# Kernel tuning notes

Measured on AMD Instinct MI355X. Metric: run time of the kernel, lower is better.

## Reference

```python
import jax, jax.numpy as jnp
import numpy as np

NEG_SLOPE = 0.2
EPS = 1e-16

N_NODES = 10000
N_EDGES = 80000
F_IN = 128
HID = 300
H1 = 5  # first_heads
H3 = 3  # out_head
N_CLASSES = 40


def gat_conv(x, edge_index, W, att_src, att_dst, bias, heads, out_ch, concat):
    """PyG-style GATConv (v1 attention), eval mode (no dropout).

    x: [N, F_in]; edge_index: [2, E] (row 0 = source, row 1 = target),
    self-loops already included. W: [F_in, heads*out_ch];
    att_src/att_dst: [heads, out_ch].
    """
    N = x.shape[0]
    h = (x @ W).reshape(N, heads, out_ch)            # [N, H, C]
    a_src = jnp.einsum('nhc,hc->nh', h, att_src)     # [N, H]
    a_dst = jnp.einsum('nhc,hc->nh', h, att_dst)     # [N, H]
    src, dst = edge_index[0], edge_index[1]
    e = jax.nn.leaky_relu(a_src[src] + a_dst[dst], NEG_SLOPE)  # [E, H]
    # segment softmax over incoming edges of each target node
    m = jax.ops.segment_max(e, dst, num_segments=N)  # [N, H]
    ex = jnp.exp(e - m[dst])
    s = jax.ops.segment_sum(ex, dst, num_segments=N)
    alpha = ex / (s[dst] + EPS)                      # [E, H]
    msg = h[src] * alpha[:, :, None]                 # [E, H, C]
    out = jax.ops.segment_sum(msg, dst, num_segments=N)  # [N, H, C]
    if concat:
        out = out.reshape(N, heads * out_ch)
    else:
        out = out.mean(axis=1)
    return out + bias


def setup_inputs() -> dict:
    key = jax.random.key(0)
    ks = jax.random.split(key, 12)
    glorot = lambda k, shape: jax.random.normal(k, shape, jnp.float32) * np.sqrt(
        2.0 / (shape[0] + shape[-1]))
    x = jax.random.normal(ks[0], (N_NODES, F_IN), jnp.float32)
    edge_index = jax.random.randint(ks[1], (2, N_EDGES), 0, N_NODES, jnp.int64)
    return {
        'x': x,
        'edge_index': edge_index,
        'W1': glorot(ks[2], (F_IN, H1 * HID)),
        'as1': glorot(ks[3], (H1, HID)),
        'ad1': glorot(ks[4], (H1, HID)),
        'b1': jnp.zeros((H1 * HID,), jnp.float32),
        'W2': glorot(ks[5], (H1 * HID, H1 * HID)),
        'as2': glorot(ks[6], (H1, HID)),
        'ad2': glorot(ks[7], (H1, HID)),
        'b2': jnp.zeros((H1 * HID,), jnp.float32),
        'W3': glorot(ks[8], (H1 * HID, H3 * N_CLASSES)),
        'as3': glorot(ks[9], (H3, N_CLASSES)),
        'ad3': glorot(ks[10], (H3, N_CLASSES)),
        'b3': jnp.zeros((N_CLASSES,), jnp.float32),
    }


def reference(x, edge_index, W1, as1, ad1, b1, W2, as2, ad2, b2, W3, as3, ad3, b3):
    N = x.shape[0]
    # PyG GATConv adds self-loops by default
    loops = jnp.arange(N, dtype=edge_index.dtype)
    ei = jnp.concatenate([edge_index, jnp.stack([loops, loops])], axis=1)
    # dropout layers are identity in eval mode
    h = gat_conv(x, ei, W1, as1, ad1, b1, H1, HID, True)
    h = jax.nn.elu(h)
    h2 = gat_conv(h, ei, W2, as2, ad2, b2, H1, HID, True)
    h = jax.nn.elu(h + h2)
    h = gat_conv(h, ei, W3, as3, ad3, b3, H3, N_CLASSES, False)  # [N, n_cls]
    pooled = h.sum(axis=0, keepdims=True)                        # [1, n_cls]
    return (pooled, jax.nn.log_softmax(pooled, axis=1))
```

## Files before the change

### kernel.cpp

```cpp
#include <hip/hip_runtime.h>
#include <hip/hip_bf16.h>
#include <math.h>

#define NN       10000
#define F_IN     128
#define HID      300
#define H1       5
#define H3       3
#define NCLS     40
#define HC1      (H1*HID)
#define KPAD     1536
#define HS12     304
#define NL12     1520
#define HS3      48
#define NL3      144
#define LD3      160
#define NEG_SLOPE 0.2f
#define EPSV     1e-16f

typedef __attribute__((ext_vector_type(8))) short bf16x8;
typedef __attribute__((ext_vector_type(8))) unsigned short u16x8;
typedef __attribute__((ext_vector_type(4))) float f32x4;

__device__ inline unsigned short f2bf(float f) {
  unsigned int u = __builtin_bit_cast(unsigned int, f);
  unsigned int r = (u + 0x7FFFu + ((u >> 16) & 1u)) >> 16;
  return (unsigned short)r;
}
__device__ inline float bf2f(unsigned short s) {
  unsigned int u = ((unsigned int)s) << 16;
  return __builtin_bit_cast(float, u);
}

__device__ __forceinline__ void gl2lds16(const unsigned short* g, unsigned short* l) {
  __builtin_amdgcn_global_load_lds(
      (const __attribute__((address_space(1))) unsigned int*)(const void*)g,
      (__attribute__((address_space(3))) unsigned int*)(void*)l, 16, 0, 0);
}

__global__ void k_count(const int* __restrict__ ei, int* __restrict__ counts,
                        int E0, int Etot) {
  int e = blockIdx.x * 256 + threadIdx.x;
  if (e >= Etot) return;
  int dst = (e < E0) ? ei[E0 + e] : (e - E0);
  atomicAdd(&counts[dst], 1);
}

__global__ __launch_bounds__(256) void k_scan(const int* __restrict__ counts,
                                              int* __restrict__ offsets,
                                              int* __restrict__ cursor,
                                              int N, int Etot) {
  __shared__ int sh[256];
  const int CH = 40;
  int t = threadIdx.x;
  int base = t * CH;
  int s = 0;
  for (int i = 0; i < CH; i++) {
    int idx = base + i;
    if (idx < N) s += counts[idx];
  }
  sh[t] = s;
  __syncthreads();
  for (int d = 1; d < 256; d <<= 1) {
    int v = (t >= d) ? sh[t - d] : 0;
    __syncthreads();
    sh[t] += v;
    __syncthreads();
  }
  int run = sh[t] - s;
  for (int i = 0; i < CH; i++) {
    int idx = base + i;
    if (idx < N) {
      offsets[idx] = run;
      cursor[idx] = run;
      run += counts[idx];
    }
  }
  if (t == 0) offsets[N] = Etot;
}

__global__ void k_scatter(const int* __restrict__ ei, int* __restrict__ cursor,
                          int* __restrict__ csr_src, int E0, int Etot) {
  int e = blockIdx.x * 256 + threadIdx.x;
  if (e >= Etot) return;
  int src, dst;
  if (e < E0) { src = ei[e]; dst = ei[E0 + e]; }
  else        { src = dst = e - E0; }
  int pos = atomicAdd(&cursor[dst], 1);
  csr_src[pos] = src;
}

__global__ void k_cvt(const float* __restrict__ in, unsigned short* __restrict__ out,
                      int R, int C, int Cpad) {
  long long idx = (long long)blockIdx.x * 256 + threadIdx.x;
  if (idx >= (long long)R * Cpad) return;
  int r = (int)(idx / Cpad), c = (int)(idx - (long long)r * Cpad);
  out[idx] = (c < C) ? f2bf(in[(size_t)r * C + c]) : 0;
}

__global__ void k_attpad3(const float* __restrict__ as1, const float* __restrict__ ad1,
                          const float* __restrict__ as2, const float* __restrict__ ad2,
                          const float* __restrict__ as3, const float* __restrict__ ad3,
                          float* __restrict__ ps1, float* __restrict__ pd1,
                          float* __restrict__ ps2, float* __restrict__ pd2,
                          float* __restrict__ ps3, float* __restrict__ pd3) {
  int i = blockIdx.x * 256 + threadIdx.x;
  if (i < KPAD) {
    int h = i / HS12, cin = i - h * HS12;
    bool live = (h < H1) && (cin < HID);
    int o = live ? (h * HID + cin) : 0;
    ps1[i] = live ? as1[o] : 0.f;
    pd1[i] = live ? ad1[o] : 0.f;
    ps2[i] = live ? as2[o] : 0.f;
    pd2[i] = live ? ad2[o] : 0.f;
  }
  if (i < LD3) {
    int h = i / HS3, cin = i - h * HS3;
    bool live = (h < H3) && (cin < NCLS);
    ps3[i] = live ? as3[h * NCLS + cin] : 0.f;
    pd3[i] = live ? ad3[h * NCLS + cin] : 0.f;
  }
}

__global__ __launch_bounds__(256) void k_cvtT(const float* __restrict__ in,
                                              unsigned short* __restrict__ out,
                                              int K, int Nm, int kC, int kS, int Kp,
                                              int nC, int nS, int Nmp) {
  __shared__ float tile[64][65];
  int k0 = blockIdx.y * 64, n0 = blockIdx.x * 64;
  int c = threadIdx.x & 63, r = threadIdx.x >> 6;
  for (int rr = r; rr < 64; rr += 4) {
    int kp = k0 + rr;
    int np = n0 + c;
    float v = 0.f;
    if (kp < Kp && np < Nmp) {
      int ck = kp % kS, bk = kp / kS;
      int cn = np % nS, bn_ = np / nS;
      int ko = bk * kC + ck, no = bn_ * nC + cn;
      if (ck < kC && ko < K && cn < nC && no < Nm) v = in[(size_t)ko * Nm + no];
    }
    tile[rr][c] = v;
  }
  __syncthreads();
  for (int rr = r; rr < 64; rr += 4) {
    int np = n0 + rr, kp = k0 + c;
    if (np < Nmp && kp < Kp) out[(size_t)np * Kp + kp] = f2bf(tile[c][rr]);
  }
}

#define BM 256
#define BN 128
#define BK 64

__global__ __launch_bounds__(512) void gemm_mfma(
    const unsigned short* __restrict__ A,
    const unsigned short* __restrict__ Bt,
    unsigned short* __restrict__ Cbf,
    int M, int Kpad, int Nmat, int ldc, int klen, int nT,
    float* __restrict__ Cacc) {
  __shared__ unsigned short As[BM * BK];
  __shared__ unsigned short Bs[BN * BK];
  int tid = threadIdx.x;
  int lane = tid & 63, wid = tid >> 6;
  int wm = wid >> 1, wn = wid & 1;
  int bid = blockIdx.x;
  int slot = bid & 7, idx = bid >> 3;
  int nTi = idx % nT, mg = idx / nT;
  int bm = (slot + 8 * mg) * BM, bn = nTi * BN;
  int quad = lane >> 4, l16 = lane & 15;
  int kq = quad * 8;
  int koff = blockIdx.y * klen;

  int ar0 = min(bm + 32 * wid + l16, M - 1);
  int ar1 = min(bm + 32 * wid + 16 + l16, M - 1);
  int br0 = min(bn + 16 * wid + l16, Nmat - 1);
  const unsigned short* gA0 = A + (size_t)ar0 * Kpad + kq;
  const unsigned short* gA1 = A + (size_t)ar1 * Kpad + kq;
  const unsigned short* gB0 = Bt + (size_t)br0 * Kpad + kq;
  unsigned short* lA = As + 4 * wid * 512;
  unsigned short* lB = Bs + 2 * wid * 512;

  f32x4 acc[4][4] = {};

  for (int kt = koff; kt < koff + klen; kt += BK) {
    gl2lds16(gA0 + kt,      lA);
    gl2lds16(gA0 + kt + 32, lA + 512);
    gl2lds16(gA1 + kt,      lA + 1024);
    gl2lds16(gA1 + kt + 32, lA + 1536);
    gl2lds16(gB0 + kt,      lB);
    gl2lds16(gB0 + kt + 32, lB + 512);
    __syncthreads();
#pragma unroll
    for (int kh = 0; kh < 2; kh++) {
      bf16x8 af[4], bfr[4];
#pragma unroll
      for (int i = 0; i < 4; i++) {
        af[i]  = *(const bf16x8*)(As + ((wm * 4 + i) * 2 + kh) * 512 + lane * 8);
        bfr[i] = *(const bf16x8*)(Bs + ((wn * 4 + i) * 2 + kh) * 512 + lane * 8);
      }
#pragma unroll
      for (int i = 0; i < 4; i++)
#pragma unroll
        for (int j = 0; j < 4; j++)
          acc[i][j] = __builtin_amdgcn_mfma_f32_16x16x32_bf16(af[i], bfr[j], acc[i][j], 0, 0, 0);
    }
    __syncthreads();
  }

#pragma unroll
  for (int i = 0; i < 4; i++) {
    int rowb = bm + wm * 64 + i * 16 + quad * 4;
#pragma unroll
    for (int j = 0; j < 4; j++) {
      int col = bn + wn * 64 + j * 16 + l16;
      if (col < ldc) {
        bool live = col < Nmat;
        if (Cacc) {
#pragma unroll
          for (int r = 0; r < 4; r++) {
            int row = rowb + r;
            if (live && row < M) atomicAdd(&Cacc[(size_t)row * ldc + col], acc[i][j][r]);
          }
        } else {
#pragma unroll
          for (int r = 0; r < 4; r++) {
            int row = rowb + r;
            if (row < M) Cbf[(size_t)row * ldc + col] = live ? f2bf(acc[i][j][r]) : 0;
          }
        }
      }
    }
  }
}

__global__ void k_att(unsigned short* __restrict__ hfeat, int ldh,
                      const float* __restrict__ attp_s,
                      const float* __restrict__ attp_d,
                      float* __restrict__ asrc, float* __restrict__ adst,
                      int H, int HS, const float* __restrict__ Cacc, int Nlive) {
  int n = blockIdx.x, t = threadIdx.x;
  __shared__ float s_ps[8], s_pd[8];
  if (t < 8) { s_ps[t] = 0.f; s_pd[t] = 0.f; }
  __syncthreads();
  int col0 = t * 8;
  if (col0 < ldh) {
    int hj = col0 / HS;
    float ps = 0.f, pd = 0.f;
    if (Cacc) {
      const float4* p = (const float4*)(Cacc + (size_t)n * ldh + col0);
      float4 f0 = p[0], f1 = p[1];
      float fv[8] = {f0.x, f0.y, f0.z, f0.w, f1.x, f1.y, f1.z, f1.w};
      u16x8 st;
#pragma unroll
      for (int j = 0; j < 8; j++) {
        bool live = (col0 + j) < Nlive;
        float v = live ? fv[j] : 0.f;
        st[j] = live ? f2bf(v) : 0;
        ps += v * attp_s[col0 + j];
        pd += v * attp_d[col0 + j];
      }
      *(u16x8*)(hfeat + (size_t)n * ldh + col0) = st;
    } else {
      u16x8 rv = *(const u16x8*)(hfeat + (size_t)n * ldh + col0);
#pragma unroll
      for (int j = 0; j < 8; j++) {
        float v = bf2f(rv[j]);
        ps += v * attp_s[col0 + j];
        pd += v * attp_d[col0 + j];
      }
    }
    atomicAdd(&s_ps[hj], ps);
    atomicAdd(&s_pd[hj], pd);
  }
  __syncthreads();
  if (t < H) {
    asrc[(size_t)n * H + t] = s_ps[t];
    adst[(size_t)n * H + t] = s_pd[t];
  }
}

__global__ __launch_bounds__(64) void k_agg(
    const unsigned short* __restrict__ hfeat, int ldh,
    const float* __restrict__ asrc,
    const float* __restrict__ adst,
    const int* __restrict__ csr_src,
    const int* __restrict__ offsets,
    const float* __restrict__ bias,
    const unsigned short* __restrict__ prevbf,
    unsigned short* __restrict__ out_bf,
    const float* __restrict__ b3,
    float* __restrict__ h3,
    int HS, int C, int H, int mode) {
  int n = blockIdx.x;
  int t = threadIdx.x;
  int s0 = offsets[n], s1 = offsets[n + 1];

  __shared__ float s_ad[8], s_pm[64], s_pl[64], s_mx[8], s_rinv[8];
  __shared__ int s_src[64];
  __shared__ float s_alpha[64 * 8];
  __shared__ float s_out[LD3];

  if (t < 8) s_ad[t] = (t < H) ? adst[(size_t)n * H + t] : 0.f;
  __syncthreads();

  int hh = t & 7, sl = t >> 3;
  float m = -1e30f, l = 0.f;
  if (hh < H) {
    float ad = s_ad[hh];
    for (int p = s0 + sl; p < s1; p += 8) {
      float v = asrc[csr_src[p] * H + hh] + ad;
      v = v > 0.f ? v : NEG_SLOPE * v;
      if (v > m) { l = l * expf(m - v) + 1.f; m = v; }
      else       { l += expf(v - m); }
    }
  }
  s_pm[t] = m; s_pl[t] = l;
  __syncthreads();
  if (t < 8) {
    float M2 = -1e30f, L2 = 0.f;
    for (int k = 0; k < 8; k++) {
      float mk = s_pm[t + 8 * k], lk = s_pl[t + 8 * k];
      if (mk > M2) { L2 = L2 * expf(M2 - mk) + lk; M2 = mk; }
      else         { L2 += lk * expf(mk - M2); }
    }
    s_mx[t] = M2;
    s_rinv[t] = 1.f / (L2 + EPSV);
  }
  __syncthreads();

  int col0 = blockIdx.y * 512 + t * 8;
  bool active = col0 < ldh;
  int hj = active ? (col0 / HS) : 0;
  int cbase = col0 - hj * HS;
  float acc[8] = {};

  for (int base = s0; base < s1; base += 64) {
    int chunk = min(64, s1 - base);
    if (t < chunk) s_src[t] = csr_src[base + t];
    for (int i = t; i < chunk * 8; i += 64) {
      int e = i >> 3, h = i & 7;
      float a = 0.f;
      if (h < H) {
        float v = asrc[csr_src[base + e] * H + h] + s_ad[h];
        v = v > 0.f ? v : NEG_SLOPE * v;
        a = expf(v - s_mx[h]) * s_rinv[h];
      }
      s_alpha[i] = a;
    }
    __syncthreads();
    if (active) {
      u16x8 rv = *(const u16x8*)(hfeat + (size_t)s_src[0] * ldh + col0);
      for (int e = 0; e < chunk; e++) {
        u16x8 cur = rv;
        if (e + 1 < chunk)
          rv = *(const u16x8*)(hfeat + (size_t)s_src[e + 1] * ldh + col0);
        float al = s_alpha[e * 8 + hj];
#pragma unroll
        for (int j = 0; j < 8; j++) acc[j] += al * bf2f(cur[j]);
      }
    }
    __syncthreads();
  }

  if (mode == 2) {
    if (active) {
#pragma unroll
      for (int j = 0; j < 8; j++) s_out[col0 + j] = acc[j];
    }
    __syncthreads();
    if (t < NCLS)
      h3[(size_t)n * NCLS + t] =
          (s_out[t] + s_out[HS + t] + s_out[2 * HS + t]) * (1.f / 3.f) + b3[t];
    return;
  }

  if (!active) return;
#pragma unroll
  for (int j = 0; j < 8; j++) {
    int cin = cbase + j;
    bool live = (hj < H) && (cin < C);
    float v = 0.f;
    if (live) {
      v = acc[j] + bias[hj * C + cin];
      if (mode == 1) v += bf2f(prevbf[(size_t)n * ldh + col0 + j]);
      v = v > 0.f ? v : (expf(v) - 1.f);
    }
    out_bf[(size_t)n * ldh + col0 + j] = live ? f2bf(v) : 0;
  }
}

__global__ void k_pool(const float* __restrict__ h3, float* __restrict__ pooled,
                       int N) {
  int col = threadIdx.x;
  if (col >= NCLS) return;
  int row = blockIdx.x * 4 + threadIdx.y;
  int stride = gridDim.x * 4;
  float acc = 0.f;
  for (int r = row; r < N; r += stride) acc += h3[(size_t)r * NCLS + col];
  atomicAdd(&pooled[col], acc);
}

__global__ __launch_bounds__(64) void k_final(const float* __restrict__ pooled,
                                              float* __restrict__ out) {
  int t = threadIdx.x;
  float v = (t < NCLS) ? pooled[t] : -INFINITY;
  float m = v;
  for (int o = 32; o > 0; o >>= 1) m = fmaxf(m, __shfl_xor(m, o));
  float ex = (t < NCLS) ? expf(v - m) : 0.f;
  float s = ex;
  for (int o = 32; o > 0; o >>= 1) s += __shfl_xor(s, o);
  float lse = m + logf(s);
  if (t < NCLS) {
    out[t] = v;
    out[NCLS + t] = v - lse;
  }
}

extern "C" void kernel_launch(void* const* d_in, const int* in_sizes, int n_in,
                              void* d_out, int out_size, void* d_ws, size_t ws_size,
                              hipStream_t stream) {
  const float* x   = (const float*)d_in[0];
  const int*   ei  = (const int*)d_in[1];
  const float* W1  = (const float*)d_in[2];
  const float* as1 = (const float*)d_in[3];
  const float* ad1 = (const float*)d_in[4];
  const float* b1  = (const float*)d_in[5];
  const float* W2  = (const float*)d_in[6];
  const float* as2 = (const float*)d_in[7];
  const float* ad2 = (const float*)d_in[8];
  const float* b2  = (const float*)d_in[9];
  const float* W3  = (const float*)d_in[10];
  const float* as3 = (const float*)d_in[11];
  const float* ad3 = (const float*)d_in[12];
  const float* b3  = (const float*)d_in[13];
  float* out = (float*)d_out;

  const int N = NN;
  const int E0 = in_sizes[1] / 2;
  const int Etot = E0 + N;
  const int mT = (N + BM - 1) / BM;

  float* f = (float*)d_ws;
  float* asrc   = f;
  float* adst   = asrc + (size_t)N * H1;
  float* pooled = adst + (size_t)N * H1;
  float* h3     = pooled + 64;
  float* attps1 = h3 + (size_t)N * NCLS;
  float* attpd1 = attps1 + KPAD;
  float* attps2 = attpd1 + KPAD;
  float* attpd2 = attps2 + KPAD;
  float* attps3 = attpd2 + KPAD;
  float* attpd3 = attps3 + LD3;
  float* Cacc   = attpd3 + LD3;
  int* counts  = (int*)(Cacc + (size_t)N * LD3);
  int* offsets = counts + N;
  int* cursor  = offsets + N + 1;
  int* csr_src = cursor + N;
  uintptr_t pp = (uintptr_t)(csr_src + Etot);
  pp = (pp + 15) & ~(uintptr_t)15;
  unsigned short* hfbf = (unsigned short*)pp;
  unsigned short* abf  = hfbf + (size_t)N * KPAD;
  unsigned short* btbf = abf + (size_t)N * KPAD;

  hipMemsetAsync(counts, 0, (size_t)N * sizeof(int), stream);
  hipMemsetAsync(pooled, 0, 64 * sizeof(float), stream);

  k_count<<<(Etot + 255) / 256, 256, 0, stream>>>(ei, counts, E0, Etot);
  k_scan<<<1, 256, 0, stream>>>(counts, offsets, cursor, N, Etot);
  k_scatter<<<(Etot + 255) / 256, 256, 0, stream>>>(ei, cursor, csr_src, E0, Etot);
  k_attpad3<<<(KPAD + 255) / 256, 256, 0, stream>>>(as1, ad1, as2, ad2, as3, ad3,
                                                    attps1, attpd1, attps2, attpd2,
                                                    attps3, attpd3);

  {
    k_cvt<<<((long long)N * F_IN + 255) / 256, 256, 0, stream>>>(x, abf, N, F_IN, F_IN);
    dim3 tg((NL12 + 63) / 64, (F_IN + 63) / 64);
    k_cvtT<<<tg, 256, 0, stream>>>(W1, btbf, F_IN, HC1, F_IN, F_IN, F_IN, HID, HS12, NL12);
    int nT = (NL12 + BN - 1) / BN;
    gemm_mfma<<<dim3(nT * mT, 1), 512, 0, stream>>>(abf, btbf, hfbf, N, F_IN, NL12,
                                                    KPAD, F_IN, nT, nullptr);
    k_att<<<N, 192, 0, stream>>>(hfbf, KPAD, attps1, attpd1, asrc, adst, H1, HS12,
                                 nullptr, 0);
    k_agg<<<dim3(N, 3), 64, 0, stream>>>(hfbf, KPAD, asrc, adst, csr_src, offsets,
                                         b1, nullptr, abf, nullptr, nullptr,
                                         HS12, HID, H1, 0);
  }

  {
    dim3 tg((NL12 + 63) / 64, KPAD / 64);
    k_cvtT<<<tg, 256, 0, stream>>>(W2, btbf, HC1, HC1, HID, HS12, KPAD, HID, HS12, NL12);
    int nT = (NL12 + BN - 1) / BN;
    gemm_mfma<<<dim3(nT * mT, 1), 512, 0, stream>>>(abf, btbf, hfbf, N, KPAD, NL12,
                                                    KPAD, KPAD, nT, nullptr);
    k_att<<<N, 192, 0, stream>>>(hfbf, KPAD, attps2, attpd2, asrc, adst, H1, HS12,
                                 nullptr, 0);
    k_agg<<<dim3(N, 3), 64, 0, stream>>>(hfbf, KPAD, asrc, adst, csr_src, offsets,
                                         b2, abf, abf, nullptr, nullptr,
                                         HS12, HID, H1, 1);
  }

  {
    dim3 tg((NL3 + 63) / 64, KPAD / 64);
    k_cvtT<<<tg, 256, 0, stream>>>(W3, btbf, HC1, H3 * NCLS, HID, HS12, KPAD, NCLS, HS3, NL3);
    hipMemsetAsync(Cacc, 0, (size_t)N * LD3 * sizeof(float), stream);
    int nT = (LD3 + BN - 1) / BN;
    gemm_mfma<<<dim3(nT * mT, 4), 512, 0, stream>>>(abf, btbf, nullptr, N, KPAD, NL3,
                                                    LD3, KPAD / 4, nT, Cacc);
    k_att<<<N, 64, 0, stream>>>(hfbf, LD3, attps3, attpd3, asrc, adst, H3, HS3,
                                Cacc, NL3);
    k_agg<<<dim3(N, 1), 64, 0, stream>>>(hfbf, LD3, asrc, adst, csr_src, offsets,
                                         nullptr, nullptr, nullptr, b3, h3,
                                         HS3, NCLS, H3, 2);
  }

  k_pool<<<64, dim3(64, 4), 0, stream>>>(h3, pooled, N);
  k_final<<<1, 64, 0, stream>>>(pooled, out);
}
```

Baseline: 536.9 us.

## Split layer-2 GEMM along K into fp32 partials and fuse pooling into aggregation

The second-layer GEMM now runs with a two-way K split. Each half writes fp32 partial results to its own buffer, and the attention kernel sums and converts them to bf16. This raises the number of GEMM blocks for better CU occupancy, at the cost of much larger fp32 intermediate traffic. The final layer's per-node outputs are atomically added straight into the pooled vector, removing the h3 buffer and the separate pooling kernel, but adding contended atomics on 40 addresses.

Measured after the change: 658.5 us. 22.6% more time.

```diff
diff --git a/kernel.cpp b/kernel.cpp
--- a/kernel.cpp
+++ b/kernel.cpp
@@ -157,7 +157,7 @@
     const unsigned short* __restrict__ Bt,
     unsigned short* __restrict__ Cbf,
     int M, int Kpad, int Nmat, int ldc, int klen, int nT,
-    float* __restrict__ Cacc) {
+    float* __restrict__ Cacc, long long zstride) {
   __shared__ unsigned short As[BM * BK];
   __shared__ unsigned short Bs[BN * BK];
   int tid = threadIdx.x;
@@ -216,10 +216,19 @@
       if (col < ldc) {
         bool live = col < Nmat;
         if (Cacc) {
-#pragma unroll
-          for (int r = 0; r < 4; r++) {
-            int row = rowb + r;
-            if (live && row < M) atomicAdd(&Cacc[(size_t)row * ldc + col], acc[i][j][r]);
+          if (zstride > 0) {
+            float* dst = Cacc + (size_t)blockIdx.y * zstride;
+#pragma unroll
+            for (int r = 0; r < 4; r++) {
+              int row = rowb + r;
+              if (row < M) dst[(size_t)row * ldc + col] = acc[i][j][r];
+            }
+          } else {
+#pragma unroll
+            for (int r = 0; r < 4; r++) {
+              int row = rowb + r;
+              if (live && row < M) atomicAdd(&Cacc[(size_t)row * ldc + col], acc[i][j][r]);
+            }
           }
         } else {
 #pragma unroll
@@ -237,7 +246,9 @@
                       const float* __restrict__ attp_s,
                       const float* __restrict__ attp_d,
                       float* __restrict__ asrc, float* __restrict__ adst,
-                      int H, int HS, const float* __restrict__ Cacc, int Nlive) {
+                      int H, int HS,
+                      const float* __restrict__ Cacc,
+                      const float* __restrict__ Cacc2, int Nlive) {
   int n = blockIdx.x, t = threadIdx.x;
   __shared__ float s_ps[8], s_pd[8];
   if (t < 8) { s_ps[t] = 0.f; s_pd[t] = 0.f; }
@@ -250,6 +261,12 @@
       const float4* p = (const float4*)(Cacc + (size_t)n * ldh + col0);
       float4 f0 = p[0], f1 = p[1];
       float fv[8] = {f0.x, f0.y, f0.z, f0.w, f1.x, f1.y, f1.z, f1.w};
+      if (Cacc2) {
+        const float4* q = (const float4*)(Cacc2 + (size_t)n * ldh + col0);
+        float4 g0 = q[0], g1 = q[1];
+        fv[0] += g0.x; fv[1] += g0.y; fv[2] += g0.z; fv[3] += g0.w;
+        fv[4] += g1.x; fv[5] += g1.y; fv[6] += g1.z; fv[7] += g1.w;
+      }
       u16x8 st;
 #pragma unroll
       for (int j = 0; j < 8; j++) {
@@ -289,7 +306,7 @@
     const unsigned short* __restrict__ prevbf,
     unsigned short* __restrict__ out_bf,
     const float* __restrict__ b3,
-    float* __restrict__ h3,
+    float* __restrict__ pooled,
     int HS, int C, int H, int mode) {
   int n = blockIdx.x;
   int t = threadIdx.x;
@@ -368,9 +385,10 @@
       for (int j = 0; j < 8; j++) s_out[col0 + j] = acc[j];
     }
     __syncthreads();
-    if (t < NCLS)
-      h3[(size_t)n * NCLS + t] =
-          (s_out[t] + s_out[HS + t] + s_out[2 * HS + t]) * (1.f / 3.f) + b3[t];
+    if (t < NCLS) {
+      float v = (s_out[t] + s_out[HS + t] + s_out[2 * HS + t]) * (1.f / 3.f) + b3[t];
+      atomicAdd(&pooled[t], v);
+    }
     return;
   }
 
@@ -387,17 +405,6 @@
     }
     out_bf[(size_t)n * ldh + col0 + j] = live ? f2bf(v) : 0;
   }
-}
-
-__global__ void k_pool(const float* __restrict__ h3, float* __restrict__ pooled,
-                       int N) {
-  int col = threadIdx.x;
-  if (col >= NCLS) return;
-  int row = blockIdx.x * 4 + threadIdx.y;
-  int stride = gridDim.x * 4;
-  float acc = 0.f;
-  for (int r = row; r < N; r += stride) acc += h3[(size_t)r * NCLS + col];
-  atomicAdd(&pooled[col], acc);
 }
 
 __global__ __launch_bounds__(64) void k_final(const float* __restrict__ pooled,
@@ -439,20 +446,20 @@
   const int E0 = in_sizes[1] / 2;
   const int Etot = E0 + N;
   const int mT = (N + BM - 1) / BM;
+  const long long ZS = (long long)N * KPAD;
 
   float* f = (float*)d_ws;
   float* asrc   = f;
   float* adst   = asrc + (size_t)N * H1;
   float* pooled = adst + (size_t)N * H1;
-  float* h3     = pooled + 64;
-  float* attps1 = h3 + (size_t)N * NCLS;
+  float* attps1 = pooled + 64;
   float* attpd1 = attps1 + KPAD;
   float* attps2 = attpd1 + KPAD;
   float* attpd2 = attps2 + KPAD;
   float* attps3 = attpd2 + KPAD;
   float* attpd3 = attps3 + LD3;
   float* Cacc   = attpd3 + LD3;
-  int* counts  = (int*)(Cacc + (size_t)N * LD3);
+  int* counts  = (int*)(Cacc + 2 * (size_t)N * KPAD);
   int* offsets = counts + N;
   int* cursor  = offsets + N + 1;
   int* csr_src = cursor + N;
@@ -478,9 +485,9 @@
     k_cvtT<<<tg, 256, 0, stream>>>(W1, btbf, F_IN, HC1, F_IN, F_IN, F_IN, HID, HS12, NL12);
     int nT = (NL12 + BN - 1) / BN;
     gemm_mfma<<<dim3(nT * mT, 1), 512, 0, stream>>>(abf, btbf, hfbf, N, F_IN, NL12,
-                                                    KPAD, F_IN, nT, nullptr);
+                                                    KPAD, F_IN, nT, nullptr, 0);
     k_att<<<N, 192, 0, stream>>>(hfbf, KPAD, attps1, attpd1, asrc, adst, H1, HS12,
-                                 nullptr, 0);
+                                 nullptr, nullptr, 0);
     k_agg<<<dim3(N, 3), 64, 0, stream>>>(hfbf, KPAD, asrc, adst, csr_src, offsets,
                                          b1, nullptr, abf, nullptr, nullptr,
                                          HS12, HID, H1, 0);
@@ -490,10 +497,10 @@
     dim3 tg((NL12 + 63) / 64, KPAD / 64);
     k_cvtT<<<tg, 256, 0, stream>>>(W2, btbf, HC1, HC1, HID, HS12, KPAD, HID, HS12, NL12);
     int nT = (NL12 + BN - 1) / BN;
-    gemm_mfma<<<dim3(nT * mT, 1), 512, 0, stream>>>(abf, btbf, hfbf, N, KPAD, NL12,
-                                                    KPAD, KPAD, nT, nullptr);
+    gemm_mfma<<<dim3(nT * mT, 2), 512, 0, stream>>>(abf, btbf, nullptr, N, KPAD, NL12,
+                                                    KPAD, KPAD / 2, nT, Cacc, ZS);
     k_att<<<N, 192, 0, stream>>>(hfbf, KPAD, attps2, attpd2, asrc, adst, H1, HS12,
-                                 nullptr, 0);
+                                 Cacc, Cacc + ZS, NL12);
     k_agg<<<dim3(N, 3), 64, 0, stream>>>(hfbf, KPAD, asrc, adst, csr_src, offsets,
                                          b2, abf, abf, nullptr, nullptr,
                                          HS12, HID, H1, 1);
@@ -505,14 +512,13 @@
     hipMemsetAsync(Cacc, 0, (size_t)N * LD3 * sizeof(float), stream);
     int nT = (LD3 + BN - 1) / BN;
     gemm_mfma<<<dim3(nT * mT, 4), 512, 0, stream>>>(abf, btbf, nullptr, N, KPAD, NL3,
-                                                    LD3, KPAD / 4, nT, Cacc);
+                                                    LD3, KPAD / 4, nT, Cacc, 0);
     k_att<<<N, 64, 0, stream>>>(hfbf, LD3, attps3, attpd3, asrc, adst, H3, HS3,
-                                Cacc, NL3);
+                                Cacc, nullptr, NL3);
     k_agg<<<dim3(N, 1), 64, 0, stream>>>(hfbf, LD3, asrc, adst, csr_src, offsets,
-                                         nullptr, nullptr, nullptr, b3, h3,
+                                         nullptr, nullptr, nullptr, b3, pooled,
                                          HS3, NCLS, H3, 2);
   }
 
-  k_pool<<<64, dim3(64, 4), 0, stream>>>(h3, pooled, N);
   k_final<<<1, 64, 0, stream>>>(pooled, out);
 }
```
